# Kernel optimization log

Measured on AMD Instinct MI355X. Metric: run time of the kernel, lower is better.

## Reference

```python
import jax, jax.numpy as jnp
import numpy as np

D_MODEL = 256
D_FF = 2048
H_HEADS = 8
N_LEVELS = 5
N_POINTS = 4
SPATIAL = [(128, 128), (64, 64), (32, 32), (16, 16), (8, 8)]
LV = sum(h * w for h, w in SPATIAL)  # 21824
LQ = 900
B = 8
D_HEAD = D_MODEL // H_HEADS


def _layer_norm(x, g, b, eps=1e-5):
    m = jnp.mean(x, -1, keepdims=True)
    v = jnp.mean((x - m) ** 2, -1, keepdims=True)
    return (x - m) * jax.lax.rsqrt(v + eps) * g + b


def _ms_deform_core(value, loc, attn_w):
    # value [B,Lv,H,D]; loc [B,Lq,H,L,P,2] normalized in [0,1]; attn_w [B,Lq,H,L,P]
    Bn, Lq = loc.shape[0], loc.shape[1]
    Dh = value.shape[-1]
    out = jnp.zeros((Bn, H_HEADS, Lq, Dh), value.dtype)
    start = 0
    for l, (Hh, Ww) in enumerate(SPATIAL):
        v = value[:, start:start + Hh * Ww].transpose(0, 2, 1, 3)  # [B,H,HW,D]
        start += Hh * Ww
        xy = loc[:, :, :, l]  # [B,Lq,H,P,2]
        # grid_sample align_corners=False: pixel = norm*size - 0.5
        x = xy[..., 0] * Ww - 0.5
        y = xy[..., 1] * Hh - 0.5
        x0 = jnp.floor(x); y0 = jnp.floor(y)
        fx = x - x0; fy = y - y0
        samp = jnp.zeros((Bn, H_HEADS, Lq * N_POINTS, Dh), value.dtype)
        corners = ((0, 0, (1 - fx) * (1 - fy)), (1, 0, fx * (1 - fy)),
                   (0, 1, (1 - fx) * fy), (1, 1, fx * fy))
        for dx, dy, wgt in corners:
            xc = x0 + dx; yc = y0 + dy
            valid = (xc >= 0) & (xc < Ww) & (yc >= 0) & (yc < Hh)  # zero padding
            idx = (jnp.clip(yc, 0, Hh - 1) * Ww + jnp.clip(xc, 0, Ww - 1)).astype(jnp.int32)
            wv = jnp.where(valid, wgt, 0.0)
            idx_r = idx.transpose(0, 2, 1, 3).reshape(Bn, H_HEADS, Lq * N_POINTS)
            wv_r = wv.transpose(0, 2, 1, 3).reshape(Bn, H_HEADS, Lq * N_POINTS)
            g = jnp.take_along_axis(v, idx_r[..., None], axis=2)  # [B,H,LqP,D]
            samp = samp + wv_r[..., None] * g
        samp = samp.reshape(Bn, H_HEADS, Lq, N_POINTS, Dh)
        aw = attn_w[:, :, :, l].transpose(0, 2, 1, 3)  # [B,H,Lq,P]
        out = out + (samp * aw[..., None]).sum(axis=3)
    return out.transpose(0, 2, 1, 3).reshape(Bn, Lq, H_HEADS * Dh)


def _forward(tgt, tgt_query_pos, tgt_reference_points, memory,
             sa_w_q, sa_b_q, sa_w_k, sa_b_k, sa_w_v, sa_b_v, sa_w_o, sa_b_o,
             ca_w_off, ca_b_off, ca_w_attn, ca_b_attn, ca_w_val, ca_b_val, ca_w_out, ca_b_out,
             ffn_w1, ffn_b1, ffn_w2, ffn_b2,
             ln1_g, ln1_b, ln2_g, ln2_b, ln3_g, ln3_b):
    Lq, Bn, C = tgt.shape
    scale = float(1.0 / np.sqrt(D_HEAD))
    # ---- self-attention (torch nn.MultiheadAttention, seq-first) ----
    qk = tgt + tgt_query_pos
    def heads(x):
        return x.reshape(Lq, Bn, H_HEADS, D_HEAD).transpose(1, 2, 0, 3)
    q = heads(qk @ sa_w_q + sa_b_q) * scale
    k = heads(qk @ sa_w_k + sa_b_k)
    v = heads(tgt @ sa_w_v + sa_b_v)
    attn = jax.nn.softmax(jnp.einsum('bhqd,bhkd->bhqk', q, k), axis=-1)
    o = jnp.einsum('bhqk,bhkd->bhqd', attn, v).transpose(2, 0, 1, 3).reshape(Lq, Bn, C)
    tgt = _layer_norm(tgt + (o @ sa_w_o + sa_b_o), ln2_g, ln2_b)
    # ---- multi-scale deformable cross-attention ----
    qb = (tgt + tgt_query_pos).transpose(1, 0, 2)            # [B,Lq,C]
    ref = tgt_reference_points.transpose(1, 0, 2, 3)         # [B,Lq,L,2]
    value = (memory.transpose(1, 0, 2) @ ca_w_val + ca_b_val).reshape(Bn, LV, H_HEADS, D_HEAD)
    off = (qb @ ca_w_off + ca_b_off).reshape(Bn, Lq, H_HEADS, N_LEVELS, N_POINTS, 2)
    aw = jax.nn.softmax((qb @ ca_w_attn + ca_b_attn).reshape(Bn, Lq, H_HEADS, N_LEVELS * N_POINTS), axis=-1)
    aw = aw.reshape(Bn, Lq, H_HEADS, N_LEVELS, N_POINTS)
    offset_normalizer = jnp.asarray([[w, h] for h, w in SPATIAL], tgt.dtype)  # (W,H) per level
    loc = ref[:, :, None, :, None, :] + off / offset_normalizer[None, None, None, :, None, :]
    samp = _ms_deform_core(value, loc, aw)                   # [B,Lq,C]
    o = (samp @ ca_w_out + ca_b_out).transpose(1, 0, 2)
    tgt = _layer_norm(tgt + o, ln1_g, ln1_b)
    # ---- FFN ----
    h = jax.nn.relu(tgt @ ffn_w1 + ffn_b1)
    tgt = _layer_norm(tgt + (h @ ffn_w2 + ffn_b2), ln3_g, ln3_b)
    return tgt


def setup_inputs() -> dict:
    key = jax.random.key(0)
    ks = iter(jax.random.split(key, 64))
    f32 = jnp.float32
    def nrm(shape, s=1.0):
        return (s * jax.random.normal(next(ks), shape)).astype(f32)
    inp = {}
    inp['tgt'] = nrm((LQ, B, D_MODEL))
    inp['tgt_query_pos'] = nrm((LQ, B, D_MODEL))
    inp['tgt_reference_points'] = jax.random.uniform(next(ks), (LQ, B, N_LEVELS, 2), f32)
    inp['memory'] = nrm((LV, B, D_MODEL))
    inp['memory_spatial_shapes'] = jnp.asarray(SPATIAL, jnp.int32)
    inp['memory_level_start_index'] = jnp.asarray(np.cumsum([0] + [h * w for h, w in SPATIAL[:-1]]), jnp.int32)
    for n, shp in [('sa_w_q', (D_MODEL, D_MODEL)), ('sa_w_k', (D_MODEL, D_MODEL)),
                   ('sa_w_v', (D_MODEL, D_MODEL)), ('sa_w_o', (D_MODEL, D_MODEL)),
                   ('ca_w_off', (D_MODEL, H_HEADS * N_LEVELS * N_POINTS * 2)),
                   ('ca_w_attn', (D_MODEL, H_HEADS * N_LEVELS * N_POINTS)),
                   ('ca_w_val', (D_MODEL, D_MODEL)), ('ca_w_out', (D_MODEL, D_MODEL)),
                   ('ffn_w1', (D_MODEL, D_FF)), ('ffn_w2', (D_FF, D_MODEL))]:
        inp[n] = nrm(shp, 0.02)
    for n, d in [('sa_b_q', D_MODEL), ('sa_b_k', D_MODEL), ('sa_b_v', D_MODEL), ('sa_b_o', D_MODEL),
                 ('ca_b_off', H_HEADS * N_LEVELS * N_POINTS * 2), ('ca_b_attn', H_HEADS * N_LEVELS * N_POINTS),
                 ('ca_b_val', D_MODEL), ('ca_b_out', D_MODEL), ('ffn_b1', D_FF), ('ffn_b2', D_MODEL)]:
        inp[n] = jnp.zeros((d,), f32)
    for n in ['ln1', 'ln2', 'ln3']:
        inp[n + '_g'] = jnp.ones((D_MODEL,), f32)
        inp[n + '_b'] = jnp.zeros((D_MODEL,), f32)
    return inp


def reference(tgt, tgt_query_pos, tgt_reference_points, memory,
              memory_spatial_shapes, memory_level_start_index,
              sa_w_q, sa_b_q, sa_w_k, sa_b_k, sa_w_v, sa_b_v, sa_w_o, sa_b_o,
              ca_w_off, ca_b_off, ca_w_attn, ca_b_attn, ca_w_val, ca_b_val, ca_w_out, ca_b_out,
              ffn_w1, ffn_b1, ffn_w2, ffn_b2,
              ln1_g, ln1_b, ln2_g, ln2_b, ln3_g, ln3_b):
    # spatial shapes / level start index are static metadata (SPATIAL), kept for API parity
    return _forward(tgt, tgt_query_pos, tgt_reference_points, memory,
                    sa_w_q, sa_b_q, sa_w_k, sa_b_k, sa_w_v, sa_b_v, sa_w_o, sa_b_o,
                    ca_w_off, ca_b_off, ca_w_attn, ca_b_attn, ca_w_val, ca_b_val, ca_w_out, ca_b_out,
                    ffn_w1, ffn_b1, ffn_w2, ffn_b2,
                    ln1_g, ln1_b, ln2_g, ln2_b, ln3_g, ln3_b)
```

## Files before the change

kernel.cpp:

```cpp
#include <hip/hip_runtime.h>
#include <hip/hip_bf16.h>
#include <type_traits>

#define LQ    900
#define BSZ   8
#define ROWS  (LQ*BSZ)
#define CDIM  256
#define QKS   512
#define OAS   480
#define NH    8
#define DH    32
#define LVTOT 21824
#define VROWS (LVTOT*BSZ)
#define DFF   2048

typedef unsigned short u16;
typedef short short8 __attribute__((ext_vector_type(8)));
typedef float f32x4 __attribute__((ext_vector_type(4)));

__device__ __forceinline__ u16 f2bf(float f) {
    __hip_bfloat16 h = __float2bfloat16(f);
    return *reinterpret_cast<u16*>(&h);
}

#define SWZ(r) (((r) & 3) ^ (((r) >> 2) & 3))

__global__ __launch_bounds__(256) void wt_kernel(const float* __restrict__ W, u16* __restrict__ Wt,
                                                 int K, int N) {
    __shared__ float t[32][33];
    const int n0 = blockIdx.x * 32, k0 = blockIdx.y * 32;
    const int tx = threadIdx.x & 31, ty = threadIdx.x >> 5;
    #pragma unroll
    for (int r = ty; r < 32; r += 8)
        t[r][tx] = W[(size_t)(k0 + r) * N + n0 + tx];
    __syncthreads();
    #pragma unroll
    for (int r = ty; r < 32; r += 8)
        Wt[(size_t)(n0 + r) * K + k0 + tx] = f2bf(t[tx][r]);
}

struct Wt6 { const float* s0; const float* s1; const float* s2; const float* s3; const float* s4; const float* s5;
             u16* d0; u16* d1; u16* d2; u16* d3; u16* d4; u16* d5; };
__global__ __launch_bounds__(256) void wt6_kernel(Wt6 a) {
    __shared__ float t[32][33];
    const float* W; u16* Wt;
    switch (blockIdx.z) {
        case 0: W = a.s0; Wt = a.d0; break;
        case 1: W = a.s1; Wt = a.d1; break;
        case 2: W = a.s2; Wt = a.d2; break;
        case 3: W = a.s3; Wt = a.d3; break;
        case 4: W = a.s4; Wt = a.d4; break;
        default: W = a.s5; Wt = a.d5; break;
    }
    const int n0 = blockIdx.x * 32, k0 = blockIdx.y * 32;
    const int tx = threadIdx.x & 31, ty = threadIdx.x >> 5;
    #pragma unroll
    for (int r = ty; r < 32; r += 8)
        t[r][tx] = W[(size_t)(k0 + r) * 256 + n0 + tx];
    __syncthreads();
    #pragma unroll
    for (int r = ty; r < 32; r += 8)
        Wt[(size_t)(n0 + r) * 256 + k0 + tx] = f2bf(t[tx][r]);
}

__global__ __launch_bounds__(256) void biascat_kernel(const float* bq, const float* bk, float* bqk,
                                                      const float* boff, const float* batt, float* boa) {
    int t = blockIdx.x * 256 + threadIdx.x;
    if (t < 256) bqk[t] = bq[t];
    else if (t < 512) bqk[t] = bk[t - 256];
    else if (t < 832) boa[t - 512] = boff[t - 512];
    else if (t < 992) boa[t - 832 + 320] = batt[t - 832];
}

__device__ __forceinline__ void stage_lds(const u16* __restrict__ src, u16* dst,
                                          int row0, int K, int k0, int maxrow, int tid) {
    #pragma unroll
    for (int i = 0; i < 2; ++i) {
        const int gi = i*256 + tid;
        const int row = gi >> 2, c = gi & 3;
        int grow = row0 + row; if (grow > maxrow) grow = maxrow;
        const int sw = c ^ SWZ(row);
        const u16* gsrc = src + (size_t)grow * K + k0 + sw * 8;
        u16* ldst = dst + ((i*256 + (tid & 192)) << 3);
        __builtin_amdgcn_global_load_lds((const __attribute__((address_space(1))) void*)gsrc,
                                         (__attribute__((address_space(3))) void*)ldst, 16, 0, 0);
    }
}

template<int ADD>
__device__ __forceinline__ void load_A16(float* f, const float* __restrict__ A,
                                         const float* __restrict__ A2,
                                         int arow, int K, int k0, int aoff) {
    const float4* src = reinterpret_cast<const float4*>(&A[(size_t)arow * K + k0 + aoff]);
    float4 v[4];
    #pragma unroll
    for (int i = 0; i < 4; ++i) v[i] = src[i];
    if (ADD) {
        const float4* s2 = reinterpret_cast<const float4*>(&A2[(size_t)arow * K + k0 + aoff]);
        #pragma unroll
        for (int i = 0; i < 4; ++i) {
            float4 g = s2[i];
            v[i].x += g.x; v[i].y += g.y; v[i].z += g.z; v[i].w += g.w;
        }
    }
    #pragma unroll
    for (int i = 0; i < 4; ++i) {
        f[i*4+0] = v[i].x; f[i*4+1] = v[i].y; f[i*4+2] = v[i].z; f[i*4+3] = v[i].w;
    }
}

__device__ __forceinline__ void write_A16(u16* Adst, const float* f, int sr, int scb) {
    u16 t[16];
    #pragma unroll
    for (int i = 0; i < 16; ++i) t[i] = f2bf(f[i]);
    #pragma unroll
    for (int c4 = 0; c4 < 2; ++c4) {
        const int c = scb + c4;
        *reinterpret_cast<uint4*>(&Adst[sr*32 + ((c ^ SWZ(sr)) * 8)]) =
            *reinterpret_cast<const uint4*>(&t[c4*8]);
    }
}

template<typename AT, int RELU, int ADD, typename OutT>
__global__ __launch_bounds__(256) void gemm_mfma(const AT* __restrict__ A,
                                                 const float* __restrict__ A2,
                                                 const u16* __restrict__ Wt,
                                                 const float* __restrict__ bias,
                                                 OutT* __restrict__ C,
                                                 int M, int N, int K) {
    __shared__ __align__(16) u16 S[16384];
    const int tid = threadIdx.x;
    const int m0 = blockIdx.y * 128, n0 = blockIdx.x * 128;
    const int lane = tid & 63;
    const int wr = (tid >> 7) & 1, wc = (tid >> 6) & 1;
    const int lr = lane & 15, lg = lane >> 4;
    const int sr = tid >> 1;
    const int scb = (tid & 1) * 2;
    const int aoff = scb * 8;
    const int nsteps = K >> 5;
    const int arow = (m0 + sr < M) ? (m0 + sr) : (M - 1);

    f32x4 acc[4][4] = {};
    float fa[16];

    stage_lds(Wt, S + 8192, n0, K, 0, N - 1, tid);
    if constexpr (std::is_same<AT, float>::value) {
        load_A16<ADD>(fa, A, A2, arow, K, 0, aoff);
        write_A16(S, fa, sr, scb);
    } else {
        stage_lds((const u16*)A, S, m0, K, 0, M - 1, tid);
    }
    __syncthreads();

    for (int t = 0; t < nsteps; ++t) {
        u16* Ac = S + ((t & 1) << 12);
        u16* Bc = S + 8192 + ((t & 1) << 12);
        const int nxt = (t + 1) & 1;
        if (t + 1 < nsteps) {
            stage_lds(Wt, S + 8192 + (nxt << 12), n0, K, (t + 1) << 5, N - 1, tid);
            if constexpr (std::is_same<AT, float>::value)
                load_A16<ADD>(fa, A, A2, arow, K, (t + 1) << 5, aoff);
            else
                stage_lds((const u16*)A, S + (nxt << 12), m0, K, (t + 1) << 5, M - 1, tid);
        }
        short8 af[4], bfr[4];
        #pragma unroll
        for (int i = 0; i < 4; ++i) {
            const int r = wr*64 + i*16 + lr;
            af[i] = *reinterpret_cast<const short8*>(&Ac[r*32 + ((lg ^ SWZ(r)) * 8)]);
        }
        #pragma unroll
        for (int j = 0; j < 4; ++j) {
            const int r = wc*64 + j*16 + lr;
            bfr[j] = *reinterpret_cast<const short8*>(&Bc[r*32 + ((lg ^ SWZ(r)) * 8)]);
        }
        #pragma unroll
        for (int i = 0; i < 4; ++i)
            #pragma unroll
            for (int j = 0; j < 4; ++j)
                acc[i][j] = __builtin_amdgcn_mfma_f32_16x16x32_bf16(af[i], bfr[j], acc[i][j], 0, 0, 0);
        if (t + 1 < nsteps) {
            if constexpr (std::is_same<AT, float>::value)
                write_A16(S + (nxt << 12), fa, sr, scb);
        }
        __syncthreads();
    }

    if constexpr (std::is_same<OutT, float>::value) {
        #pragma unroll
        for (int j = 0; j < 4; ++j) {
            const int col = n0 + wc*64 + j*16 + lr;
            if (col >= N) continue;
            const float bcol = bias[col];
            #pragma unroll
            for (int i = 0; i < 4; ++i) {
                #pragma unroll
                for (int r = 0; r < 4; ++r) {
                    const int row = m0 + wr*64 + i*16 + lg*4 + r;
                    if (row >= M) continue;
                    float v = acc[i][j][r] + bcol;
                    if (RELU) v = fmaxf(v, 0.f);
                    C[(size_t)row * N + col] = v;
                }
            }
        }
    } else {
        u16* Ct = S;
        #pragma unroll
        for (int j = 0; j < 4; ++j) {
            const int col = wc*64 + j*16 + lr;
            const float bcol = bias[n0 + col];
            #pragma unroll
            for (int i = 0; i < 4; ++i)
                #pragma unroll
                for (int r = 0; r < 4; ++r) {
                    float v = acc[i][j][r] + bcol;
                    if (RELU) v = fmaxf(v, 0.f);
                    Ct[(wr*64 + i*16 + lg*4 + r)*128 + col] = f2bf(v);
                }
        }
        __syncthreads();
        #pragma unroll
        for (int it = 0; it < 8; ++it) {
            const int idx = it*256 + tid;
            const int row = idx >> 4, cc = idx & 15;
            if (m0 + row < M)
                *reinterpret_cast<uint4*>(&C[(size_t)(m0 + row) * N + n0 + cc*8]) =
                    *reinterpret_cast<const uint4*>(&Ct[row*128 + cc*8]);
        }
    }
}

__global__ __launch_bounds__(256) void attn_mfma_kernel(const float* __restrict__ qk,
                                                        const float* __restrict__ v,
                                                        float* __restrict__ out) {
    __shared__ __align__(16) u16 Ks[64*32];
    __shared__ __align__(16) u16 Vt[32*64];
    const int bx = blockIdx.x;
    const int qt = bx & 7, h = (bx >> 3) & 7, b = bx >> 6;
    const int tid = threadIdx.x;
    const int w = tid >> 6, lane = tid & 63;
    const int lr = lane & 15, lg = lane >> 4;
    const int m0 = qt*128 + w*32;
    const float scale = 0.1767766952966369f;

    short8 qf[2];
    #pragma unroll
    for (int j = 0; j < 2; ++j) {
        int lq = m0 + j*16 + lr; if (lq > LQ-1) lq = LQ-1;
        const float* qp = &qk[((size_t)lq*BSZ + b)*QKS + h*DH + lg*8];
        float4 a = *reinterpret_cast<const float4*>(qp);
        float4 c = *reinterpret_cast<const float4*>(qp + 4);
        u16 t[8] = { f2bf(a.x*scale), f2bf(a.y*scale), f2bf(a.z*scale), f2bf(a.w*scale),
                     f2bf(c.x*scale), f2bf(c.y*scale), f2bf(c.z*scale), f2bf(c.w*scale) };
        qf[j] = *reinterpret_cast<short8*>(t);
    }

    f32x4 o00 = {}, o01 = {}, o10 = {}, o11 = {};
    float m[2] = {-1e30f, -1e30f}, l[2] = {0.f, 0.f};
    const f32x4 zero = {};

    for (int kt = 0; kt < 15; ++kt) {
        __syncthreads();
        {
            const int key = tid >> 2, c = tid & 3;
            int kg = kt*64 + key; if (kg > LQ-1) kg = LQ-1;
            const size_t kbase = ((size_t)kg*BSZ + b)*QKS + 256 + h*DH + c*8;
            const size_t vbase = ((size_t)kg*BSZ + b)*CDIM + h*DH + c*8;
            float4 k0 = *reinterpret_cast<const float4*>(&qk[kbase]);
            float4 k1 = *reinterpret_cast<const float4*>(&qk[kbase+4]);
            float4 v0 = *reinterpret_cast<const float4*>(&v[vbase]);
            float4 v1 = *reinterpret_cast<const float4*>(&v[vbase+4]);
            u16 kb[8] = { f2bf(k0.x), f2bf(k0.y), f2bf(k0.z), f2bf(k0.w),
                          f2bf(k1.x), f2bf(k1.y), f2bf(k1.z), f2bf(k1.w) };
            *reinterpret_cast<short8*>(&Ks[key*32 + ((c ^ ((key>>1)&3)) * 8)]) =
                *reinterpret_cast<short8*>(kb);
            float vv[8] = { v0.x, v0.y, v0.z, v0.w, v1.x, v1.y, v1.z, v1.w };
            #pragma unroll
            for (int e = 0; e < 8; ++e) {
                const int dh = c*8 + e;
                Vt[dh*64 + (((key>>3) ^ (dh&7)) * 8) + (key&7)] = f2bf(vv[e]);
            }
        }
        __syncthreads();

        f32x4 s[4][2];
        #pragma unroll
        for (int i = 0; i < 4; ++i) {
            const int key = i*16 + lr;
            short8 kf = *reinterpret_cast<const short8*>(&Ks[key*32 + ((lg ^ ((key>>1)&3)) * 8)]);
            s[i][0] = __builtin_amdgcn_mfma_f32_16x16x32_bf16(kf, qf[0], zero, 0, 0, 0);
            s[i][1] = __builtin_amdgcn_mfma_f32_16x16x32_bf16(kf, qf[1], zero, 0, 0, 0);
        }
        const int lim = LQ - kt*64 - lg*4;
        #pragma unroll
        for (int i = 0; i < 4; ++i)
            #pragma unroll
            for (int r = 0; r < 4; ++r)
                if (i*16 + r >= lim) { s[i][0][r] = -1e30f; s[i][1][r] = -1e30f; }

        #pragma unroll
        for (int j = 0; j < 2; ++j) {
            float mx = -1e30f;
            #pragma unroll
            for (int i = 0; i < 4; ++i)
                #pragma unroll
                for (int r = 0; r < 4; ++r) mx = fmaxf(mx, s[i][j][r]);
            mx = fmaxf(mx, __shfl_xor(mx, 16));
            mx = fmaxf(mx, __shfl_xor(mx, 32));
            const float mn = fmaxf(m[j], mx);
            const float corr = __expf(m[j] - mn);
            float sum = 0.f;
            #pragma unroll
            for (int i = 0; i < 4; ++i)
                #pragma unroll
                for (int r = 0; r < 4; ++r) {
                    float p = __expf(s[i][j][r] - mn);
                    s[i][j][r] = p;
                    sum += p;
                }
            sum += __shfl_xor(sum, 16);
            sum += __shfl_xor(sum, 32);
            l[j] = l[j]*corr + sum;
            m[j] = mn;
            if (j == 0) { o00 *= corr; o10 *= corr; }
            else        { o01 *= corr; o11 *= corr; }
        }

        short8 pb[2][2];
        #pragma unroll
        for (int kh = 0; kh < 2; ++kh)
            #pragma unroll
            for (int j = 0; j < 2; ++j) {
                u16 t[8];
                #pragma unroll
                for (int e = 0; e < 4; ++e) {
                    t[e]   = f2bf(s[2*kh][j][e]);
                    t[e+4] = f2bf(s[2*kh+1][j][e]);
                }
                pb[kh][j] = *reinterpret_cast<short8*>(t);
            }

        #pragma unroll
        for (int ip = 0; ip < 2; ++ip) {
            const int dh = ip*16 + lr;
            #pragma unroll
            for (int kh = 0; kh < 2; ++kh) {
                u16 t[8];
                const int c0 = (kh*4 + (lg>>1)) ^ (dh&7);
                const int c1 = (kh*4 + 2 + (lg>>1)) ^ (dh&7);
                *reinterpret_cast<uint2*>(&t[0]) =
                    *reinterpret_cast<const uint2*>(&Vt[dh*64 + c0*8 + (lg&1)*4]);
                *reinterpret_cast<uint2*>(&t[4]) =
                    *reinterpret_cast<const uint2*>(&Vt[dh*64 + c1*8 + (lg&1)*4]);
                short8 vf = *reinterpret_cast<short8*>(t);
                if (ip == 0) {
                    o00 = __builtin_amdgcn_mfma_f32_16x16x32_bf16(vf, pb[kh][0], o00, 0, 0, 0);
                    o01 = __builtin_amdgcn_mfma_f32_16x16x32_bf16(vf, pb[kh][1], o01, 0, 0, 0);
                } else {
                    o10 = __builtin_amdgcn_mfma_f32_16x16x32_bf16(vf, pb[kh][0], o10, 0, 0, 0);
                    o11 = __builtin_amdgcn_mfma_f32_16x16x32_bf16(vf, pb[kh][1], o11, 0, 0, 0);
                }
            }
        }
    }

    #pragma unroll
    for (int j = 0; j < 2; ++j) {
        const int lq = m0 + j*16 + lr;
        if (lq >= LQ) continue;
        const float inv = 1.f / l[j];
        float* op = &out[((size_t)lq*BSZ + b)*CDIM + h*DH];
        #pragma unroll
        for (int r = 0; r < 4; ++r) {
            const f32x4& a0 = (j == 0) ? o00 : o01;
            const f32x4& a1 = (j == 0) ? o10 : o11;
            op[lg*4 + r]      = a0[r] * inv;
            op[16 + lg*4 + r] = a1[r] * inv;
        }
    }
}

__global__ __launch_bounds__(256) void ln_res_kernel(const float* __restrict__ xin,
                                                     const float* __restrict__ res,
                                                     const float* __restrict__ g,
                                                     const float* __restrict__ beta,
                                                     float* __restrict__ out) {
    const int row  = blockIdx.x * 4 + (threadIdx.x >> 6);
    const int lane = threadIdx.x & 63;
    const size_t base = (size_t)row * CDIM + lane * 4;
    float4 a = *reinterpret_cast<const float4*>(&xin[base]);
    float4 r = *reinterpret_cast<const float4*>(&res[base]);
    float x0 = a.x+r.x, x1 = a.y+r.y, x2 = a.z+r.z, x3 = a.w+r.w;
    float s = x0+x1+x2+x3;
    #pragma unroll
    for (int o = 1; o < 64; o <<= 1) s += __shfl_xor(s, o);
    float mean = s * (1.f/256.f);
    float d0 = x0-mean, d1 = x1-mean, d2 = x2-mean, d3 = x3-mean;
    float sq = d0*d0 + d1*d1 + d2*d2 + d3*d3;
    #pragma unroll
    for (int o = 1; o < 64; o <<= 1) sq += __shfl_xor(sq, o);
    float rs = rsqrtf(sq * (1.f/256.f) + 1e-5f);
    float4 gg = *reinterpret_cast<const float4*>(&g[lane*4]);
    float4 bb = *reinterpret_cast<const float4*>(&beta[lane*4]);
    float4 o4 = make_float4(d0*rs*gg.x+bb.x, d1*rs*gg.y+bb.y, d2*rs*gg.z+bb.z, d3*rs*gg.w+bb.w);
    *reinterpret_cast<float4*>(&out[base]) = o4;
}

__global__ __launch_bounds__(256) void softmax20_kernel(float* __restrict__ oab) {
    int item = blockIdx.x * 256 + threadIdx.x;
    if (item >= ROWS * NH) return;
    int row = item >> 3, h = item & 7;
    float* p = &oab[(size_t)row*OAS + 320 + h*20];
    float mx = -1e30f;
    float e[20];
    #pragma unroll
    for (int j = 0; j < 20; ++j) mx = fmaxf(mx, p[j]);
    float sum = 0.f;
    #pragma unroll
    for (int j = 0; j < 20; ++j) { e[j] = __expf(p[j] - mx); sum += e[j]; }
    float inv = 1.f / sum;
    #pragma unroll
    for (int j = 0; j < 20; ++j) p[j] = e[j] * inv;
}

__global__ __launch_bounds__(256) void msdeform_kernel(const u16* __restrict__ value,
                                                       const float* __restrict__ oab,
                                                       const float* __restrict__ refp,
                                                       float* __restrict__ samp) {
    const int gid = blockIdx.x * 32 + (threadIdx.x >> 3);
    const int ch  = (threadIdx.x & 7) * 4;
    const int h   = gid & 7;
    const int row = gid >> 3;
    const int b   = row & 7;
    const int WL[5] = {128, 64, 32, 16, 8};
    const int SL[5] = {0, 16384, 20480, 21504, 21760};
    const u16* vbase = value + h*DH + ch;
    float a0 = 0.f, a1 = 0.f, a2 = 0.f, a3 = 0.f;
    #pragma unroll
    for (int l = 0; l < 5; ++l) {
        const float2 r2 = *reinterpret_cast<const float2*>(&refp[((size_t)row*5 + l)*2]);
        const int W = WL[l];
        const float Wf = (float)W;
        #pragma unroll
        for (int p = 0; p < 4; ++p) {
            const float2 o2 = *reinterpret_cast<const float2*>(&oab[(size_t)row*OAS + ((h*5 + l)*4 + p)*2]);
            const float aw = oab[(size_t)row*OAS + 320 + h*20 + l*4 + p];
            const float x = (r2.x + o2.x / Wf) * Wf - 0.5f;
            const float y = (r2.y + o2.y / Wf) * Wf - 0.5f;
            const float x0f = floorf(x), y0f = floorf(y);
            const float fx = x - x0f, fy = y - y0f;
            const int x0 = (int)x0f, y0 = (int)y0f;
            float wx0 = (1.f - fx) * aw, wx1 = fx * aw;
            float fy0 = 1.f - fy, fy1 = fy;
            if (x0 < 0 || x0 >= W)       wx0 = 0.f;
            if (x0+1 < 0 || x0+1 >= W)   wx1 = 0.f;
            if (y0 < 0 || y0 >= W)       fy0 = 0.f;
            if (y0+1 < 0 || y0+1 >= W)   fy1 = 0.f;
            const float w00 = wx0*fy0, w10 = wx1*fy0, w01 = wx0*fy1, w11 = wx1*fy1;
            const int xc0 = min(max(x0, 0), W-1),   xc1 = min(max(x0+1, 0), W-1);
            const int yc0 = min(max(y0, 0), W-1),   yc1 = min(max(y0+1, 0), W-1);
            const int r0 = SL[l] + yc0*W, r1 = SL[l] + yc1*W;
            const int o00i = ((r0 + xc0)*BSZ + b) * CDIM;
            const int o10i = ((r0 + xc1)*BSZ + b) * CDIM;
            const int o01i = ((r1 + xc0)*BSZ + b) * CDIM;
            const int o11i = ((r1 + xc1)*BSZ + b) * CDIM;
            const uint2 u00 = *reinterpret_cast<const uint2*>(vbase + o00i);
            const uint2 u10 = *reinterpret_cast<const uint2*>(vbase + o10i);
            const uint2 u01 = *reinterpret_cast<const uint2*>(vbase + o01i);
            const uint2 u11 = *reinterpret_cast<const uint2*>(vbase + o11i);
            a0 += w00 * __uint_as_float(u00.x << 16) + w10 * __uint_as_float(u10.x << 16)
                + w01 * __uint_as_float(u01.x << 16) + w11 * __uint_as_float(u11.x << 16);
            a1 += w00 * __uint_as_float(u00.x & 0xffff0000u) + w10 * __uint_as_float(u10.x & 0xffff0000u)
                + w01 * __uint_as_float(u01.x & 0xffff0000u) + w11 * __uint_as_float(u11.x & 0xffff0000u);
            a2 += w00 * __uint_as_float(u00.y << 16) + w10 * __uint_as_float(u10.y << 16)
                + w01 * __uint_as_float(u01.y << 16) + w11 * __uint_as_float(u11.y << 16);
            a3 += w00 * __uint_as_float(u00.y & 0xffff0000u) + w10 * __uint_as_float(u10.y & 0xffff0000u)
                + w01 * __uint_as_float(u01.y & 0xffff0000u) + w11 * __uint_as_float(u11.y & 0xffff0000u);
        }
    }
    float4 o4 = make_float4(a0, a1, a2, a3);
    *reinterpret_cast<float4*>(&samp[(size_t)row*CDIM + h*DH + ch]) = o4;
}

extern "C" void kernel_launch(void* const* d_in, const int* in_sizes, int n_in,
                              void* d_out, int out_size, void* d_ws, size_t ws_size,
                              hipStream_t stream) {
    (void)in_sizes; (void)n_in; (void)out_size; (void)ws_size;
    const float* tgt    = (const float*)d_in[0];
    const float* qpos   = (const float*)d_in[1];
    const float* refpts = (const float*)d_in[2];
    const float* memory = (const float*)d_in[3];
    const float* Wq  = (const float*)d_in[6];
    const float* Wk  = (const float*)d_in[7];
    const float* Wv  = (const float*)d_in[8];
    const float* Wo  = (const float*)d_in[9];
    const float* Woff= (const float*)d_in[10];
    const float* Watt= (const float*)d_in[11];
    const float* Wval= (const float*)d_in[12];
    const float* Wout= (const float*)d_in[13];
    const float* W1  = (const float*)d_in[14];
    const float* W2  = (const float*)d_in[15];
    const float* bq  = (const float*)d_in[16];
    const float* bk  = (const float*)d_in[17];
    const float* bv  = (const float*)d_in[18];
    const float* bo  = (const float*)d_in[19];
    const float* boff= (const float*)d_in[20];
    const float* batt= (const float*)d_in[21];
    const float* bval= (const float*)d_in[22];
    const float* bout= (const float*)d_in[23];
    const float* b1  = (const float*)d_in[24];
    const float* b2  = (const float*)d_in[25];
    const float* ln1g= (const float*)d_in[26];
    const float* ln1b= (const float*)d_in[27];
    const float* ln2g= (const float*)d_in[28];
    const float* ln2b= (const float*)d_in[29];
    const float* ln3g= (const float*)d_in[30];
    const float* ln3b= (const float*)d_in[31];
    float* out = (float*)d_out;

    char* ws = (char*)d_ws;
    const size_t RB = (size_t)ROWS * CDIM * 4;
    float* tgt2  = (float*)(ws + 0*RB);
    float* tgt3  = (float*)(ws + 1*RB);
    float* qk    = (float*)(ws + 2*RB);
    float* vbuf  = (float*)(ws + 3*RB);
    float* abuf  = (float*)(ws + 4*RB);
    float* qkbuf = (float*)(ws + 5*RB);
    float* oab   = (float*)(ws + 5*RB + (size_t)ROWS*QKS*4);
    char*  wsm   = ws + 5*RB + (size_t)ROWS*QKS*4 + (size_t)ROWS*OAS*4;
    u16* WqkT  = (u16*)(wsm);
    u16* WvT   = (u16*)(wsm + 262144);
    u16* WoT   = (u16*)(wsm + 262144 + 1*131072);
    u16* WvalT = (u16*)(wsm + 262144 + 2*131072);
    u16* WoutT = (u16*)(wsm + 262144 + 3*131072);
    u16* WoaT  = (u16*)(wsm + 262144 + 4*131072);
    float* bqk = (float*)(wsm + 2*262144 + 4*131072);
    float* boa = (float*)(wsm + 2*262144 + 4*131072 + 2048);
    char* big  = wsm + 2*262144 + 4*131072 + 4096;
    u16* valb  = (u16*)big;
    u16* W1T   = (u16*)big;
    u16* W2T   = (u16*)(big + 1048576);
    u16* ffnh  = (u16*)(big + 2097152);

    const dim3 blk(256);

    Wt6 wargs = { Wq, Wk, Wv, Wo, Wval, Wout,
                  WqkT, WqkT + 256*256, WvT, WoT, WvalT, WoutT };
    wt6_kernel<<<dim3(8,8,6), blk, 0, stream>>>(wargs);
    wt_kernel<<<dim3(10,8), blk, 0, stream>>>(Woff, WoaT, CDIM, 320);
    wt_kernel<<<dim3(5,8),  blk, 0, stream>>>(Watt, WoaT + 320*256, CDIM, 160);
    biascat_kernel<<<dim3(4), blk, 0, stream>>>(bq, bk, bqk, boff, batt, boa);

    gemm_mfma<float,0,1,float><<<dim3(4,57), blk, 0, stream>>>(tgt, qpos, WqkT, bqk, qkbuf, ROWS, QKS, CDIM);
    gemm_mfma<float,0,0,float><<<dim3(2,57), blk, 0, stream>>>(tgt, nullptr, WvT, bv, vbuf, ROWS, CDIM, CDIM);
    attn_mfma_kernel<<<dim3(512), blk, 0, stream>>>(qkbuf, vbuf, abuf);
    gemm_mfma<float,0,0,float><<<dim3(2,57), blk, 0, stream>>>(abuf, nullptr, WoT, bo, qk, ROWS, CDIM, CDIM);
    ln_res_kernel<<<dim3(ROWS/4), blk, 0, stream>>>(qk, tgt, ln2g, ln2b, tgt2);

    gemm_mfma<float,0,0,u16><<<dim3(2,1364), blk, 0, stream>>>(memory, nullptr, WvalT, bval, valb, VROWS, CDIM, CDIM);
    gemm_mfma<float,0,1,float><<<dim3(4,57), blk, 0, stream>>>(tgt2, qpos, WoaT, boa, oab, ROWS, OAS, CDIM);
    softmax20_kernel<<<dim3((ROWS*NH+255)/256), blk, 0, stream>>>(oab);
    msdeform_kernel<<<dim3(ROWS*NH/32), blk, 0, stream>>>(valb, oab, refpts, vbuf);
    gemm_mfma<float,0,0,float><<<dim3(2,57), blk, 0, stream>>>(vbuf, nullptr, WoutT, bout, qk, ROWS, CDIM, CDIM);
    ln_res_kernel<<<dim3(ROWS/4), blk, 0, stream>>>(qk, tgt2, ln1g, ln1b, tgt3);

    wt_kernel<<<dim3(64,8), blk, 0, stream>>>(W1, W1T, CDIM, DFF);
    wt_kernel<<<dim3(8,64), blk, 0, stream>>>(W2, W2T, DFF, CDIM);
    gemm_mfma<float,1,0,u16><<<dim3(16,57), blk, 0, stream>>>(tgt3, nullptr, W1T, b1, ffnh, ROWS, DFF, CDIM);
    gemm_mfma<u16,0,0,float><<<dim3(2,57),  blk, 0, stream>>>((const u16*)ffnh, nullptr, W2T, b2, abuf, ROWS, CDIM, DFF);
    ln_res_kernel<<<dim3(ROWS/4), blk, 0, stream>>>(abuf, tgt3, ln3g, ln3b, out);
}
```

Measured before the change: 387.9 us.

## Merge weight prep into one kernel and batch value/QK/V GEMMs with bf16 outputs

All weight transposes and bias concatenations, including the FFN weights, now run in a single prep kernel. The attention scale is folded into Wq and bq, so it no longer has to be applied in the attention kernel. The memory-value, QK and V projections run as one grouped GEMM launch that writes bf16 outputs, and the attention kernel reads those bf16 buffers directly. This cuts launch count, lets the small GEMMs fill gaps alongside the large value GEMM, and halves QK/V traffic, at the cost of rearranging the workspace layout.

```diff
diff --git a/kernel.cpp b/kernel.cpp
--- a/kernel.cpp
+++ b/kernel.cpp
@@ -24,52 +24,46 @@
 }
 
 #define SWZ(r) (((r) & 3) ^ (((r) >> 2) & 3))
-
-__global__ __launch_bounds__(256) void wt_kernel(const float* __restrict__ W, u16* __restrict__ Wt,
-                                                 int K, int N) {
+#define ATTN_SCALE 0.1767766952966369f
+
+struct PrepArgs {
+    const float* Wq; const float* Wk; const float* Wv; const float* Wo;
+    const float* Wval; const float* Wout; const float* Woff; const float* Watt;
+    const float* W1; const float* W2;
+    u16* WqkT; u16* WvT; u16* WoT; u16* WvalT; u16* WoutT; u16* WoaT; u16* W1T; u16* W2T;
+    const float* bq; const float* bk; const float* boff; const float* batt;
+    float* bqk; float* boa;
+};
+__global__ __launch_bounds__(256) void prep_kernel(PrepArgs a) {
     __shared__ float t[32][33];
-    const int n0 = blockIdx.x * 32, k0 = blockIdx.y * 32;
+    const int id = blockIdx.x;
+    if (id == 1528) {
+        const int tx = threadIdx.x;
+        if (tx < 256) { a.bqk[tx] = a.bq[tx] * ATTN_SCALE; a.bqk[256 + tx] = a.bk[tx]; }
+        for (int i = tx; i < 320; i += 256) a.boa[i] = a.boff[i];
+        if (tx < 160) a.boa[320 + tx] = a.batt[tx];
+        return;
+    }
+    const float* W; u16* Wt; int K = 256, N = 256, nx = 8; float scale = 1.f; int r;
+    if      (id < 64)   { W = a.Wq;   Wt = a.WqkT;           scale = ATTN_SCALE; r = id; }
+    else if (id < 128)  { W = a.Wk;   Wt = a.WqkT + 256*256; r = id - 64; }
+    else if (id < 192)  { W = a.Wv;   Wt = a.WvT;            r = id - 128; }
+    else if (id < 256)  { W = a.Wo;   Wt = a.WoT;            r = id - 192; }
+    else if (id < 320)  { W = a.Wval; Wt = a.WvalT;          r = id - 256; }
+    else if (id < 384)  { W = a.Wout; Wt = a.WoutT;          r = id - 320; }
+    else if (id < 464)  { W = a.Woff; Wt = a.WoaT;           N = 320; nx = 10; r = id - 384; }
+    else if (id < 504)  { W = a.Watt; Wt = a.WoaT + 320*256; N = 160; nx = 5;  r = id - 464; }
+    else if (id < 1016) { W = a.W1;   Wt = a.W1T;            N = 2048; nx = 64; r = id - 504; }
+    else                { W = a.W2;   Wt = a.W2T;            K = 2048; N = 256; nx = 8; r = id - 1016; }
+    const int n0 = (r % nx) * 32, k0 = (r / nx) * 32;
     const int tx = threadIdx.x & 31, ty = threadIdx.x >> 5;
     #pragma unroll
-    for (int r = ty; r < 32; r += 8)
-        t[r][tx] = W[(size_t)(k0 + r) * N + n0 + tx];
+    for (int rr = ty; rr < 32; rr += 8)
+        t[rr][tx] = W[(size_t)(k0 + rr) * N + n0 + tx];
     __syncthreads();
     #pragma unroll
-    for (int r = ty; r < 32; r += 8)
-        Wt[(size_t)(n0 + r) * K + k0 + tx] = f2bf(t[tx][r]);
-}
-
-struct Wt6 { const float* s0; const float* s1; const float* s2; const float* s3; const float* s4; const float* s5;
-             u16* d0; u16* d1; u16* d2; u16* d3; u16* d4; u16* d5; };
-__global__ __launch_bounds__(256) void wt6_kernel(Wt6 a) {
-    __shared__ float t[32][33];
-    const float* W; u16* Wt;
-    switch (blockIdx.z) {
-        case 0: W = a.s0; Wt = a.d0; break;
-        case 1: W = a.s1; Wt = a.d1; break;
-        case 2: W = a.s2; Wt = a.d2; break;
-        case 3: W = a.s3; Wt = a.d3; break;
-        case 4: W = a.s4; Wt = a.d4; break;
-        default: W = a.s5; Wt = a.d5; break;
-    }
-    const int n0 = blockIdx.x * 32, k0 = blockIdx.y * 32;
-    const int tx = threadIdx.x & 31, ty = threadIdx.x >> 5;
-    #pragma unroll
-    for (int r = ty; r < 32; r += 8)
-        t[r][tx] = W[(size_t)(k0 + r) * 256 + n0 + tx];
-    __syncthreads();
-    #pragma unroll
-    for (int r = ty; r < 32; r += 8)
-        Wt[(size_t)(n0 + r) * 256 + k0 + tx] = f2bf(t[tx][r]);
-}
-
-__global__ __launch_bounds__(256) void biascat_kernel(const float* bq, const float* bk, float* bqk,
-                                                      const float* boff, const float* batt, float* boa) {
-    int t = blockIdx.x * 256 + threadIdx.x;
-    if (t < 256) bqk[t] = bq[t];
-    else if (t < 512) bqk[t] = bk[t - 256];
-    else if (t < 832) boa[t - 512] = boff[t - 512];
-    else if (t < 992) boa[t - 832 + 320] = batt[t - 832];
+    for (int rr = ty; rr < 32; rr += 8)
+        Wt[(size_t)(n0 + rr) * K + k0 + tx] = f2bf(t[tx][rr] * scale);
 }
 
 __device__ __forceinline__ void stage_lds(const u16* __restrict__ src, u16* dst,
@@ -87,15 +81,14 @@
     }
 }
 
-template<int ADD>
-__device__ __forceinline__ void load_A16(float* f, const float* __restrict__ A,
-                                         const float* __restrict__ A2,
-                                         int arow, int K, int k0, int aoff) {
+__device__ __forceinline__ void load_A16r(float* f, const float* __restrict__ A,
+                                          const float* __restrict__ A2,
+                                          int arow, int K, int k0, int aoff) {
     const float4* src = reinterpret_cast<const float4*>(&A[(size_t)arow * K + k0 + aoff]);
     float4 v[4];
     #pragma unroll
     for (int i = 0; i < 4; ++i) v[i] = src[i];
-    if (ADD) {
+    if (A2) {
         const float4* s2 = reinterpret_cast<const float4*>(&A2[(size_t)arow * K + k0 + aoff]);
         #pragma unroll
         for (int i = 0; i < 4; ++i) {
@@ -118,6 +111,87 @@
         const int c = scb + c4;
         *reinterpret_cast<uint4*>(&Adst[sr*32 + ((c ^ SWZ(sr)) * 8)]) =
             *reinterpret_cast<const uint4*>(&t[c4*8]);
+    }
+}
+
+__global__ __launch_bounds__(256) void mgemm3_kernel(
+        const float* __restrict__ Aval, const u16* __restrict__ WvalT, const float* __restrict__ bval, u16* __restrict__ Cval,
+        const float* __restrict__ Aqk,  const float* __restrict__ Aqk2, const u16* __restrict__ WqkT,
+        const float* __restrict__ bqk,  u16* __restrict__ Cqk,
+        const float* __restrict__ Av,   const u16* __restrict__ WvT,   const float* __restrict__ bv, u16* __restrict__ Cv) {
+    __shared__ __align__(16) u16 S[16384];
+    const int tid = threadIdx.x;
+    int id = blockIdx.x;
+    const float *A, *A2 = nullptr; const u16* Wt; const float* bias; u16* C; int M, N, bx, by;
+    if (id < 2728)      { A = Aval; Wt = WvalT; bias = bval; C = Cval; M = VROWS; N = 256; bx = id & 1; by = id >> 1; }
+    else if (id < 2956) { id -= 2728; A = Aqk; A2 = Aqk2; Wt = WqkT; bias = bqk; C = Cqk; M = ROWS; N = 512; bx = id & 3; by = id >> 2; }
+    else                { id -= 2956; A = Av; Wt = WvT; bias = bv; C = Cv; M = ROWS; N = 256; bx = id & 1; by = id >> 1; }
+    const int m0 = by * 128, n0 = bx * 128;
+    const int lane = tid & 63;
+    const int wr = (tid >> 7) & 1, wc = (tid >> 6) & 1;
+    const int lr = lane & 15, lg = lane >> 4;
+    const int sr = tid >> 1;
+    const int scb = (tid & 1) * 2;
+    const int aoff = scb * 8;
+    const int arow = (m0 + sr < M) ? (m0 + sr) : (M - 1);
+
+    f32x4 acc[4][4] = {};
+    float fa[16];
+
+    stage_lds(Wt, S + 8192, n0, 256, 0, N - 1, tid);
+    load_A16r(fa, A, A2, arow, 256, 0, aoff);
+    write_A16(S, fa, sr, scb);
+    __syncthreads();
+
+    #pragma unroll
+    for (int t = 0; t < 8; ++t) {
+        u16* Ac = S + ((t & 1) << 12);
+        u16* Bc = S + 8192 + ((t & 1) << 12);
+        const int nxt = (t + 1) & 1;
+        if (t + 1 < 8) {
+            stage_lds(Wt, S + 8192 + (nxt << 12), n0, 256, (t + 1) << 5, N - 1, tid);
+            load_A16r(fa, A, A2, arow, 256, (t + 1) << 5, aoff);
+        }
+        short8 af[4], bfr[4];
+        #pragma unroll
+        for (int i = 0; i < 4; ++i) {
+            const int r = wr*64 + i*16 + lr;
+            af[i] = *reinterpret_cast<const short8*>(&Ac[r*32 + ((lg ^ SWZ(r)) * 8)]);
+        }
+        #pragma unroll
+        for (int j = 0; j < 4; ++j) {
+            const int r = wc*64 + j*16 + lr;
+            bfr[j] = *reinterpret_cast<const short8*>(&Bc[r*32 + ((lg ^ SWZ(r)) * 8)]);
+        }
+        #pragma unroll
+        for (int i = 0; i < 4; ++i)
+            #pragma unroll
+            for (int j = 0; j < 4; ++j)
+                acc[i][j] = __builtin_amdgcn_mfma_f32_16x16x32_bf16(af[i], bfr[j], acc[i][j], 0, 0, 0);
+        if (t + 1 < 8)
+            write_A16(S + (nxt << 12), fa, sr, scb);
+        __syncthreads();
+    }
+
+    u16* Ct = S;
+    #pragma unroll
+    for (int j = 0; j < 4; ++j) {
+        const int col = wc*64 + j*16 + lr;
+        const float bcol = bias[n0 + col];
+        #pragma unroll
+        for (int i = 0; i < 4; ++i)
+            #pragma unroll
+            for (int r = 0; r < 4; ++r)
+                Ct[(wr*64 + i*16 + lg*4 + r)*128 + col] = f2bf(acc[i][j][r] + bcol);
+    }
+    __syncthreads();
+    #pragma unroll
+    for (int it = 0; it < 8; ++it) {
+        const int idx = it*256 + tid;
+        const int row = idx >> 4, cc = idx & 15;
+        if (m0 + row < M)
+            *reinterpret_cast<uint4*>(&C[(size_t)(m0 + row) * N + n0 + cc*8]) =
+                *reinterpret_cast<const uint4*>(&Ct[row*128 + cc*8]);
     }
 }
 
@@ -145,7 +219,7 @@
 
     stage_lds(Wt, S + 8192, n0, K, 0, N - 1, tid);
     if constexpr (std::is_same<AT, float>::value) {
-        load_A16<ADD>(fa, A, A2, arow, K, 0, aoff);
+        load_A16r(fa, A, ADD ? A2 : nullptr, arow, K, 0, aoff);
         write_A16(S, fa, sr, scb);
     } else {
         stage_lds((const u16*)A, S, m0, K, 0, M - 1, tid);
@@ -159,7 +233,7 @@
         if (t + 1 < nsteps) {
             stage_lds(Wt, S + 8192 + (nxt << 12), n0, K, (t + 1) << 5, N - 1, tid);
             if constexpr (std::is_same<AT, float>::value)
-                load_A16<ADD>(fa, A, A2, arow, K, (t + 1) << 5, aoff);
+                load_A16r(fa, A, ADD ? A2 : nullptr, arow, K, (t + 1) << 5, aoff);
             else
                 stage_lds((const u16*)A, S + (nxt << 12), m0, K, (t + 1) << 5, M - 1, tid);
         }
@@ -231,8 +305,8 @@
     }
 }
 
-__global__ __launch_bounds__(256) void attn_mfma_kernel(const float* __restrict__ qk,
-                                                        const float* __restrict__ v,
+__global__ __launch_bounds__(256) void attn_mfma_kernel(const u16* __restrict__ qkb,
+                                                        const u16* __restrict__ vb,
                                                         float* __restrict__ out) {
     __shared__ __align__(16) u16 Ks[64*32];
     __shared__ __align__(16) u16 Vt[32*64];
@@ -242,18 +316,12 @@
     const int w = tid >> 6, lane = tid & 63;
     const int lr = lane & 15, lg = lane >> 4;
     const int m0 = qt*128 + w*32;
-    const float scale = 0.1767766952966369f;
 
     short8 qf[2];
     #pragma unroll
     for (int j = 0; j < 2; ++j) {
         int lq = m0 + j*16 + lr; if (lq > LQ-1) lq = LQ-1;
-        const float* qp = &qk[((size_t)lq*BSZ + b)*QKS + h*DH + lg*8];
-        float4 a = *reinterpret_cast<const float4*>(qp);
-        float4 c = *reinterpret_cast<const float4*>(qp + 4);
-        u16 t[8] = { f2bf(a.x*scale), f2bf(a.y*scale), f2bf(a.z*scale), f2bf(a.w*scale),
-                     f2bf(c.x*scale), f2bf(c.y*scale), f2bf(c.z*scale), f2bf(c.w*scale) };
-        qf[j] = *reinterpret_cast<short8*>(t);
+        qf[j] = *reinterpret_cast<const short8*>(&qkb[((size_t)lq*BSZ + b)*QKS + h*DH + lg*8]);
     }
 
     f32x4 o00 = {}, o01 = {}, o10 = {}, o11 = {};
@@ -265,21 +333,14 @@
         {
             const int key = tid >> 2, c = tid & 3;
             int kg = kt*64 + key; if (kg > LQ-1) kg = LQ-1;
-            const size_t kbase = ((size_t)kg*BSZ + b)*QKS + 256 + h*DH + c*8;
-            const size_t vbase = ((size_t)kg*BSZ + b)*CDIM + h*DH + c*8;
-            float4 k0 = *reinterpret_cast<const float4*>(&qk[kbase]);
-            float4 k1 = *reinterpret_cast<const float4*>(&qk[kbase+4]);
-            float4 v0 = *reinterpret_cast<const float4*>(&v[vbase]);
-            float4 v1 = *reinterpret_cast<const float4*>(&v[vbase+4]);
-            u16 kb[8] = { f2bf(k0.x), f2bf(k0.y), f2bf(k0.z), f2bf(k0.w),
-                          f2bf(k1.x), f2bf(k1.y), f2bf(k1.z), f2bf(k1.w) };
             *reinterpret_cast<short8*>(&Ks[key*32 + ((c ^ ((key>>1)&3)) * 8)]) =
-                *reinterpret_cast<short8*>(kb);
-            float vv[8] = { v0.x, v0.y, v0.z, v0.w, v1.x, v1.y, v1.z, v1.w };
+                *reinterpret_cast<const short8*>(&qkb[((size_t)kg*BSZ + b)*QKS + 256 + h*DH + c*8]);
+            short8 vv = *reinterpret_cast<const short8*>(&vb[((size_t)kg*BSZ + b)*CDIM + h*DH + c*8]);
+            const u16* pv = reinterpret_cast<const u16*>(&vv);
             #pragma unroll
             for (int e = 0; e < 8; ++e) {
                 const int dh = c*8 + e;
-                Vt[dh*64 + (((key>>3) ^ (dh&7)) * 8) + (key&7)] = f2bf(vv[e]);
+                Vt[dh*64 + (((key>>3) ^ (dh&7)) * 8) + (key&7)] = pv[e];
             }
         }
         __syncthreads();
@@ -526,48 +587,47 @@
     float* qk    = (float*)(ws + 2*RB);
     float* vbuf  = (float*)(ws + 3*RB);
     float* abuf  = (float*)(ws + 4*RB);
-    float* qkbuf = (float*)(ws + 5*RB);
-    float* oab   = (float*)(ws + 5*RB + (size_t)ROWS*QKS*4);
-    char*  wsm   = ws + 5*RB + (size_t)ROWS*QKS*4 + (size_t)ROWS*OAS*4;
+    u16* qkb = (u16*)(ws + 5*RB);
+    u16* vb  = (u16*)(ws + 5*RB + (size_t)ROWS*QKS*2);
+    float* oab = (float*)(ws + 5*RB + (size_t)ROWS*QKS*2 + (size_t)ROWS*CDIM*2);
+    char* wsm = ws + 5*RB + (size_t)ROWS*QKS*2 + (size_t)ROWS*CDIM*2 + (size_t)ROWS*OAS*4;
     u16* WqkT  = (u16*)(wsm);
     u16* WvT   = (u16*)(wsm + 262144);
     u16* WoT   = (u16*)(wsm + 262144 + 1*131072);
     u16* WvalT = (u16*)(wsm + 262144 + 2*131072);
     u16* WoutT = (u16*)(wsm + 262144 + 3*131072);
     u16* WoaT  = (u16*)(wsm + 262144 + 4*131072);
-    float* bqk = (float*)(wsm + 2*262144 + 4*131072);
-    float* boa = (float*)(wsm + 2*262144 + 4*131072 + 2048);
-    char* big  = wsm + 2*262144 + 4*131072 + 4096;
+    u16* W1T   = (u16*)(wsm + 2*262144 + 4*131072);
+    u16* W2T   = (u16*)(wsm + 2*262144 + 4*131072 + 1048576);
+    float* bqk = (float*)(wsm + 2*262144 + 4*131072 + 2097152);
+    float* boa = (float*)(wsm + 2*262144 + 4*131072 + 2097152 + 2048);
+    char* big  = wsm + 2*262144 + 4*131072 + 2097152 + 4096;
     u16* valb  = (u16*)big;
-    u16* W1T   = (u16*)big;
-    u16* W2T   = (u16*)(big + 1048576);
-    u16* ffnh  = (u16*)(big + 2097152);
+    u16* ffnh  = (u16*)(big + (size_t)VROWS*CDIM*2);
 
     const dim3 blk(256);
 
-    Wt6 wargs = { Wq, Wk, Wv, Wo, Wval, Wout,
-                  WqkT, WqkT + 256*256, WvT, WoT, WvalT, WoutT };
-    wt6_kernel<<<dim3(8,8,6), blk, 0, stream>>>(wargs);
-    wt_kernel<<<dim3(10,8), blk, 0, stream>>>(Woff, WoaT, CDIM, 320);
-    wt_kernel<<<dim3(5,8),  blk, 0, stream>>>(Watt, WoaT + 320*256, CDIM, 160);
-    biascat_kernel<<<dim3(4), blk, 0, stream>>>(bq, bk, bqk, boff, batt, boa);
-
-    gemm_mfma<float,0,1,float><<<dim3(4,57), blk, 0, stream>>>(tgt, qpos, WqkT, bqk, qkbuf, ROWS, QKS, CDIM);
-    gemm_mfma<float,0,0,float><<<dim3(2,57), blk, 0, stream>>>(tgt, nullptr, WvT, bv, vbuf, ROWS, CDIM, CDIM);
-    attn_mfma_kernel<<<dim3(512), blk, 0, stream>>>(qkbuf, vbuf, abuf);
+    PrepArgs pa = { Wq, Wk, Wv, Wo, Wval, Wout, Woff, Watt, W1, W2,
+                    WqkT, WvT, WoT, WvalT, WoutT, WoaT, W1T, W2T,
+                    bq, bk, boff, batt, bqk, boa };
+    prep_kernel<<<dim3(1529), blk, 0, stream>>>(pa);
+
+    mgemm3_kernel<<<dim3(3070), blk, 0, stream>>>(
+        memory, WvalT, bval, valb,
+        tgt, qpos, WqkT, bqk, qkb,
+        tgt, WvT, bv, vb);
+
+    attn_mfma_kernel<<<dim3(512), blk, 0, stream>>>(qkb, vb, abuf);
     gemm_mfma<float,0,0,float><<<dim3(2,57), blk, 0, stream>>>(abuf, nullptr, WoT, bo, qk, ROWS, CDIM, CDIM);
     ln_res_kernel<<<dim3(ROWS/4), blk, 0, stream>>>(qk, tgt, ln2g, ln2b, tgt2);
 
-    gemm_mfma<float,0,0,u16><<<dim3(2,1364), blk, 0, stream>>>(memory, nullptr, WvalT, bval, valb, VROWS, CDIM, CDIM);
     gemm_mfma<float,0,1,float><<<dim3(4,57), blk, 0, stream>>>(tgt2, qpos, WoaT, boa, oab, ROWS, OAS, CDIM);
     softmax20_kernel<<<dim3((ROWS*NH+255)/256), blk, 0, stream>>>(oab);
     msdeform_kernel<<<dim3(ROWS*NH/32), blk, 0, stream>>>(valb, oab, refpts, vbuf);
     gemm_mfma<float,0,0,float><<<dim3(2,57), blk, 0, stream>>>(vbuf, nullptr, WoutT, bout, qk, ROWS, CDIM, CDIM);
     ln_res_kernel<<<dim3(ROWS/4), blk, 0, stream>>>(qk, tgt2, ln1g, ln1b, tgt3);
 
-    wt_kernel<<<dim3(64,8), blk, 0, stream>>>(W1, W1T, CDIM, DFF);
-    wt_kernel<<<dim3(8,64), blk, 0, stream>>>(W2, W2T, DFF, CDIM);
     gemm_mfma<float,1,0,u16><<<dim3(16,57), blk, 0, stream>>>(tgt3, nullptr, W1T, b1, ffnh, ROWS, DFF, CDIM);
-    gemm_mfma<u16,0,0,float><<<dim3(2,57),  blk, 0, stream>>>((const u16*)ffnh, nullptr, W2T, b2, abuf, ROWS, CDIM, DFF);
+    gemm_mfma<u16,0,0,float><<<dim3(2,57),  blk, 0, stream>>>(ffnh, nullptr, W2T, b2, abuf, ROWS, CDIM, DFF);
     ln_res_kernel<<<dim3(ROWS/4), blk, 0, stream>>>(abuf, tgt3, ln3g, ln3b, out);
 }
```

New measurement: 358.2 us. 7.6% less time.
